# Kernel tuning notes

Hardware: AMD Instinct MI355X
Metric: run time of the kernel (lower is better)

## Reference

```python
import jax, jax.numpy as jnp
import numpy as np

# levels for the auction iterations: j = 7..-1 gives level = -4^j, j = -2 gives level = 0
_LEVEL_JS = list(range(7, -3, -1))


def approx_match(xyz1, xyz2):
    # xyz1: [B,N,3], xyz2: [B,M,3] -> soft match matrix [B,N,M]
    B, N, _ = xyz1.shape
    M = xyz2.shape[1]
    multiL = 1.0 if N >= M else float(M // N)
    multiR = float(N // M) if N >= M else 1.0
    # pairwise squared distances [B,N,M]
    d2 = jnp.sum((xyz1[:, :, None, :] - xyz2[:, None, :, :]) ** 2, axis=-1)
    levels = jnp.array([0.0 if j == -2 else -(4.0 ** j) for j in _LEVEL_JS],
                       dtype=xyz1.dtype)

    def step(carry, level):
        match, remainL, remainR = carry
        w = jnp.exp(level * d2) * remainR[:, None, :]                      # [B,N,M]
        # row-normalize to each left point's remaining mass
        w = w * (remainL / (jnp.sum(w, axis=2) + 1e-9))[:, :, None]
        # clip columns to right points' remaining capacity
        ss = jnp.sum(w, axis=1) + 1e-9                                     # [B,M]
        w = w * jnp.minimum(remainR / ss, 1.0)[:, None, :]
        match = match + w
        remainL = jnp.maximum(remainL - jnp.sum(w, axis=2), 0.0)
        remainR = jnp.maximum(remainR - jnp.sum(w, axis=1), 0.0)
        return (match, remainL, remainR), None

    init = (jnp.zeros_like(d2),
            jnp.full((B, N), multiL, dtype=d2.dtype),
            jnp.full((B, M), multiR, dtype=d2.dtype))
    (match, _, _), _ = jax.lax.scan(step, init, levels)
    return match


def match_cost(xyz1, xyz2, match):
    # cost[b] = sum_{k,l} match[b,k,l] * ||xyz1[b,k] - xyz2[b,l]||
    d = jnp.sqrt(jnp.sum((xyz1[:, :, None, :] - xyz2[:, None, :, :]) ** 2, axis=-1))
    return jnp.sum(match * d, axis=(1, 2))


def setup_inputs() -> dict:
    key = jax.random.key(0)
    k1, k2 = jax.random.split(key)
    B, N, M = 8, 2048, 2048
    input1 = jax.random.normal(k1, (B, N, 3), dtype=jnp.float32)
    input2 = jax.random.normal(k2, (B, M, 3), dtype=jnp.float32)
    return {"input1": input1, "input2": input2}


def reference(input1, input2):
    match = approx_match(input1, input2)
    return match_cost(input1, input2, match)
```

## Files before the change

kernel.cpp:

```cpp
#include <hip/hip_runtime.h>
#include <hip/hip_fp16.h>


#define BATCH 8
#define NPTS 2048
#define MPTS 2048
#define BLOCK 256
#define ROWS 16
#define BLOCKS_PER_BATCH 128
#define NSUB 8
#define SUBTGT (BLOCKS_PER_BATCH / NSUB)
#define NSYNC 21
#define PAD 16
#define SROW 17
#define LOG2E 1.44269504088896340736f

__device__ __forceinline__ float fast_exp2(float x) {
  return __builtin_amdgcn_exp2f(x);
}
__device__ __forceinline__ float fast_sqrt(float a) {
  return __builtin_amdgcn_sqrtf(a);
}
__device__ __forceinline__ float packh2(float c, float r) {
  __half2 h = __halves2half2(__float2half_rn(c), __float2half_rn(r));
  return __builtin_bit_cast(float, h);
}

__device__ __forceinline__ float cohLoad(const float* p) {
  return __hip_atomic_load((float*)p, __ATOMIC_RELAXED,
                           __HIP_MEMORY_SCOPE_AGENT);
}
__device__ __forceinline__ void cohStore(float* p, float v) {
  __hip_atomic_store(p, v, __ATOMIC_RELAXED, __HIP_MEMORY_SCOPE_AGENT);
}
__device__ __forceinline__ float4 cohLoad4(const float4* p) {
  const float* f = (const float*)p;
  return make_float4(cohLoad(f), cohLoad(f + 1), cohLoad(f + 2),
                     cohLoad(f + 3));
}

__device__ __forceinline__ void lds_barrier() {
  asm volatile("s_waitcnt lgkmcnt(0)" ::: "memory");
  __builtin_amdgcn_s_barrier();
  __builtin_amdgcn_sched_barrier(0);
}

__device__ __forceinline__ void batch_barrier(unsigned* base, int bid) {
  __syncthreads();
  if (threadIdx.x == 0) {
    __hip_atomic_fetch_add(base + (bid & (NSUB - 1)) * PAD, 1u,
                           __ATOMIC_RELAXED, __HIP_MEMORY_SCOPE_AGENT);
  }
  if (threadIdx.x < NSUB) {
    int guard = 0;
    while (__hip_atomic_load(base + threadIdx.x * PAD, __ATOMIC_RELAXED,
                             __HIP_MEMORY_SCOPE_AGENT) < (unsigned)SUBTGT) {
      __builtin_amdgcn_s_sleep(2);
      if (++guard > (1 << 22)) break;
    }
  }
  asm volatile("" ::: "memory");
  __syncthreads();
}

__device__ __forceinline__ void load8(const float4* q, int r0,
                                      float* x, float* y, float* z) {
  int b4 = (r0 >> 2) * 3;
  float4 q0 = q[b4], q1 = q[b4 + 1], q2 = q[b4 + 2];
  float4 q3 = q[b4 + 3], q4 = q[b4 + 4], q5 = q[b4 + 5];
  x[0] = q0.x; y[0] = q0.y; z[0] = q0.z;
  x[1] = q0.w; y[1] = q1.x; z[1] = q1.y;
  x[2] = q1.z; y[2] = q1.w; z[2] = q2.x;
  x[3] = q2.y; y[3] = q2.z; z[3] = q2.w;
  x[4] = q3.x; y[4] = q3.y; z[4] = q3.z;
  x[5] = q3.w; y[5] = q4.x; z[5] = q4.y;
  x[6] = q4.z; y[6] = q4.w; z[6] = q5.x;
  x[7] = q5.y; y[7] = q5.z; z[7] = q5.w;
}

__device__ __forceinline__ void sweep2T_fuse(
    float nc, int tid, int t0, const float4* q1, const float* rsG,
    float* wpB, const float4* sP, float4* sStage4, float* sRR) {
  const int m_idx = tid >> 4, c = tid & 15;
  const float4 pm = sP[t0 + m_idx];
  const float4* rsg4 = (const float4*)rsG;
  const int rowb = c * SROW;
  const bool isXyz = tid < 192;
  const int t = tid - 192;
  const int wIdx = isXyz ? ((tid / 12) * SROW + (tid % 12))
                         : ((t >> 2) * SROW + 12 + (t & 3));
  float4 v = isXyz ? q1[tid] : cohLoad4(rsg4 + t);
  float part = 0.f;
  for (int chunk = 0; chunk < 8; ++chunk) {
    lds_barrier();
    sStage4[wIdx] = v;
    if (chunk < 7) {
      v = isXyz ? q1[(chunk + 1) * 192 + tid]
                : cohLoad4(rsg4 + (chunk + 1) * 64 + t);
    }
    lds_barrier();
#pragma unroll
    for (int k = 0; k < 4; ++k) {
      float4 a  = sStage4[rowb + 3 * k];
      float4 bb = sStage4[rowb + 3 * k + 1];
      float4 cc = sStage4[rowb + 3 * k + 2];
      float4 r4 = sStage4[rowb + 12 + k];
      float px[4] = {a.x, a.w, bb.z, cc.y};
      float py[4] = {a.y, bb.x, bb.w, cc.z};
      float pz[4] = {a.z, bb.y, cc.x, cc.w};
      float rr[4] = {r4.x, r4.y, r4.z, r4.w};
#pragma unroll
      for (int j = 0; j < 4; ++j) {
        float dx = px[j] - pm.x, dy = py[j] - pm.y, dz = pz[j] - pm.z;
        float d2 = __builtin_fmaf(dx, dx, __builtin_fmaf(dy, dy, dz * dz));
        part = __builtin_fmaf(fast_exp2(nc * d2), rr[j], part);
      }
    }
  }
  part += __shfl_xor(part, 1, 64);
  part += __shfl_xor(part, 2, 64);
  part += __shfl_xor(part, 4, 64);
  part += __shfl_xor(part, 8, 64);
  if (c == 0) {
    float t1v = part;
    float rr = sRR[m_idx];
    float colsum = rr * t1v;
    float cs = fminf(rr / (colsum + 1e-9f), 1.0f);
    float ccv = rr * cs;
    float rn = fmaxf(rr - colsum * cs, 0.f);
    cohStore(wpB + t0 + m_idx, packh2(ccv, rn));
    sRR[m_idx] = rn;
  }
}

__global__ __launch_bounds__(BLOCK, 4) void emd_fused_kernel(
    const float* __restrict__ xyz1, const float* __restrict__ xyz2,
    float* __restrict__ out, float* __restrict__ rowscaleG,
    float* __restrict__ wPack, float* __restrict__ R9acc,
    float* __restrict__ t9, float* __restrict__ outAcc,
    unsigned* __restrict__ ctr) {
  __shared__ float4 sP[MPTS];
  __shared__ float4 sStage4[16 * SROW];
  __shared__ float sRedS[ROWS * 4];
  __shared__ float sRedC[ROWS * 4];
  __shared__ float sRedR[ROWS * 4];
  __shared__ float sCost[ROWS];
  __shared__ float sRowScale[ROWS];
  __shared__ float sRemainL[ROWS];
  __shared__ float sRR[ROWS];

  const int tid = threadIdx.x;
  const int bid = blockIdx.x;
  const int b = bid >> 7;
  const int t0 = (bid & 127) * ROWS;
  const bool desig = (bid & 127) == 0;
  const int wave = tid >> 6, lane = tid & 63;
  const size_t bM = (size_t)b * MPTS;
  float costAcc = 0.f;

  float* rsG = rowscaleG + (size_t)b * NPTS;
  float* wpB = wPack + bM;
  const float4* q1 = (const float4*)(xyz1 + (size_t)b * NPTS * 3);
  const float4* q2 = (const float4*)(xyz2 + bM * 3);
#define CTRB(s) (ctr + (size_t)(((s) * BATCH + b) * NSUB) * PAD)

  for (int g = tid; g < MPTS / 4; g += BLOCK) {
    float4 a = q2[3 * g], bb = q2[3 * g + 1], c = q2[3 * g + 2];
    sP[4 * g + 0] = make_float4(a.x, a.y, a.z, 0.f);
    sP[4 * g + 1] = make_float4(a.w, bb.x, bb.y, 0.f);
    sP[4 * g + 2] = make_float4(bb.z, bb.w, c.x, 0.f);
    sP[4 * g + 3] = make_float4(c.y, c.z, c.w, 0.f);
  }
  if (tid < ROWS) sRR[tid] = 1.0f;
  if (desig && tid == 0) {
    cohStore(R9acc + b * PAD, 0.f);
    cohStore(t9 + b * PAD, 0.f);
    cohStore(outAcc + b * PAD, 0.f);
  }
  __syncthreads();

  const float nc0 = -16384.0f * LOG2E;
  {
    const int ph = lane >> 1, rg = lane & 1;
    float x1a[8], y1a[8], z1a[8], acc[8];
    load8(q1, t0 + rg * 8, x1a, y1a, z1a);
#pragma unroll
    for (int j = 0; j < 8; ++j) acc[j] = 0.f;
    const int mb = wave * 512 + ph;
#pragma unroll 2
    for (int it = 0; it < 16; ++it) {
      float4 v = sP[mb + it * 32];
#pragma unroll
      for (int j = 0; j < 8; ++j) {
        float dx = x1a[j] - v.x, dy = y1a[j] - v.y, dz = z1a[j] - v.z;
        float d2 = __builtin_fmaf(dx, dx, __builtin_fmaf(dy, dy, dz * dz));
        acc[j] += fast_exp2(nc0 * d2);
      }
    }
#pragma unroll
    for (int j = 0; j < 8; ++j) {
      acc[j] += __shfl_xor(acc[j], 2, 64);
      acc[j] += __shfl_xor(acc[j], 4, 64);
      acc[j] += __shfl_xor(acc[j], 8, 64);
      acc[j] += __shfl_xor(acc[j], 16, 64);
      acc[j] += __shfl_xor(acc[j], 32, 64);
    }
    if (lane < 2) {
#pragma unroll
      for (int j = 0; j < 8; ++j) sRedS[(rg * 8 + j) * 4 + wave] = acc[j];
    }
    __syncthreads();
    if (tid < ROWS) {
      float s = sRedS[tid * 4] + sRedS[tid * 4 + 1] + sRedS[tid * 4 + 2] +
                sRedS[tid * 4 + 3];
      float rs = 1.0f / (s + 1e-9f);
      sRowScale[tid] = rs;
      cohStore(rsG + t0 + tid, rs);
    }
  }
  batch_barrier(CTRB(0), bid);
  sweep2T_fuse(nc0, tid, t0, q1, rsG, wpB, sP, sStage4, sRR);
  batch_barrier(CTRB(1), bid);

  float x1[4], y1[4], z1[4];
  {
    int b4 = ((t0 + (lane & 3) * 4) >> 2) * 3;
    float4 a = q1[b4], bb = q1[b4 + 1], c = q1[b4 + 2];
    x1[0] = a.x;  y1[0] = a.y;  z1[0] = a.z;
    x1[1] = a.w;  y1[1] = bb.x; z1[1] = bb.y;
    x1[2] = bb.z; y1[2] = bb.w; z1[2] = c.x;
    x1[3] = c.y;  y1[3] = c.z;  z1[3] = c.w;
  }
  const int phc = lane >> 2, rgc = lane & 3;
  const int mbc = wave * 512 + phc;

  float nc2 = -4096.0f * LOG2E;
  for (int l = 0; l < 9; ++l) {
    const bool LAST = (l == 8);
#pragma unroll
    for (int k = 0; k < 8; ++k) {
      int m = tid + k * 256;
      sP[m].w = cohLoad(wpB + m);
    }
    __syncthreads();
    float accS[4] = {0.f, 0.f, 0.f, 0.f};
    float accC[4] = {0.f, 0.f, 0.f, 0.f};
    float accR[4] = {0.f, 0.f, 0.f, 0.f};
#pragma unroll 4
    for (int it = 0; it < 32; ++it) {
      float4 v = sP[mbc + it * 16];
      __half2 h = __builtin_bit_cast(__half2, v.w);
      float cc = __low2float(h);
      float rr = __high2float(h);
#pragma unroll
      for (int j = 0; j < 4; ++j) {
        float dx = x1[j] - v.x, dy = y1[j] - v.y, dz = z1[j] - v.z;
        float d2 = __builtin_fmaf(dx, dx, __builtin_fmaf(dy, dy, dz * dz));
        float sq = fast_sqrt(d2);
        float e2 = fast_exp2(nc2 * d2);
        float e2s = e2 * e2;
        float e1 = e2s * e2s;
        float t = e1 * cc;
        accS[j] += t;
        accC[j] = __builtin_fmaf(t, sq, accC[j]);
        accR[j] = __builtin_fmaf(e2, rr, accR[j]);
      }
    }
#pragma unroll
    for (int j = 0; j < 4; ++j) {
      accS[j] += __shfl_xor(accS[j], 4, 64);
      accS[j] += __shfl_xor(accS[j], 8, 64);
      accS[j] += __shfl_xor(accS[j], 16, 64);
      accS[j] += __shfl_xor(accS[j], 32, 64);
      accC[j] += __shfl_xor(accC[j], 4, 64);
      accC[j] += __shfl_xor(accC[j], 8, 64);
      accC[j] += __shfl_xor(accC[j], 16, 64);
      accC[j] += __shfl_xor(accC[j], 32, 64);
      accR[j] += __shfl_xor(accR[j], 4, 64);
      accR[j] += __shfl_xor(accR[j], 8, 64);
      accR[j] += __shfl_xor(accR[j], 16, 64);
      accR[j] += __shfl_xor(accR[j], 32, 64);
    }
    if (lane < 4) {
#pragma unroll
      for (int j = 0; j < 4; ++j) {
        sRedS[(rgc * 4 + j) * 4 + wave] = accS[j];
        sRedC[(rgc * 4 + j) * 4 + wave] = accC[j];
        sRedR[(rgc * 4 + j) * 4 + wave] = accR[j];
      }
    }
    __syncthreads();
    if (tid < ROWS) {
      float S2 = sRedS[tid * 4] + sRedS[tid * 4 + 1] + sRedS[tid * 4 + 2] +
                 sRedS[tid * 4 + 3];
      float C = sRedC[tid * 4] + sRedC[tid * 4 + 1] + sRedC[tid * 4 + 2] +
                sRedC[tid * 4 + 3];
      float R = sRedR[tid * 4] + sRedR[tid * 4 + 1] + sRedR[tid * 4 + 2] +
                sRedR[tid * 4 + 3];
      if (LAST) R = cohLoad(R9acc + b * PAD);
      float rs = sRowScale[tid];
      float rl = (l == 0) ? 1.0f : sRemainL[tid];
      float rlN = fmaxf(rl - rs * S2, 0.f);
      sRemainL[tid] = rlN;
      float rsN = rlN / (R + 1e-9f);
      sRowScale[tid] = rsN;
      if (!LAST) cohStore(rsG + t0 + tid, rsN);
      sCost[tid] = rs * C;
    }
    __syncthreads();
    if (tid == 0) {
      float t = 0.f;
#pragma unroll
      for (int i = 0; i < ROWS; ++i) t += sCost[i];
      costAcc += t;
      if (LAST) {
        float r = 0.f;
#pragma unroll
        for (int i = 0; i < ROWS; ++i) r += sRowScale[i];
        atomicAdd(t9 + b * PAD, r);
      }
    }
    if (!LAST) {
      batch_barrier(CTRB(2 + 2 * l), bid);
      sweep2T_fuse(nc2, tid, t0, q1, rsG, wpB, sP, sStage4, sRR);
      if (l == 7) {
        __syncthreads();
        if (tid == 0) {
          float r9 = 0.f;
#pragma unroll
          for (int i = 0; i < ROWS; ++i) r9 += sRR[i];
          atomicAdd(R9acc + b * PAD, r9);
        }
      }
      batch_barrier(CTRB(3 + 2 * l), bid);
      nc2 *= 0.25f;
    }
  }
  batch_barrier(CTRB(18), bid);

  if (tid < ROWS) {
    float rr = sRR[tid];
    float t1s = cohLoad(t9 + b * PAD);
    float w = rr * fminf(rr / (__builtin_fmaf(rr, t1s, 1e-9f)), 1.0f);
    cohStore(wpB + t0 + tid, w);
  }
  batch_barrier(CTRB(19), bid);

  {
#pragma unroll
    for (int k = 0; k < 8; ++k) {
      int m = tid + k * 256;
      sP[m].w = cohLoad(wpB + m);
    }
    __syncthreads();
    const int ph = lane >> 1, rg = lane & 1;
    float x1a[8], y1a[8], z1a[8], acc[8];
    load8(q1, t0 + rg * 8, x1a, y1a, z1a);
#pragma unroll
    for (int j = 0; j < 8; ++j) acc[j] = 0.f;
    const int mb = wave * 512 + ph;
#pragma unroll 2
    for (int it = 0; it < 16; ++it) {
      float4 v = sP[mb + it * 32];
#pragma unroll
      for (int j = 0; j < 8; ++j) {
        float dx = x1a[j] - v.x, dy = y1a[j] - v.y, dz = z1a[j] - v.z;
        float d2 = __builtin_fmaf(dx, dx, __builtin_fmaf(dy, dy, dz * dz));
        acc[j] = __builtin_fmaf(fast_sqrt(d2), v.w, acc[j]);
      }
    }
#pragma unroll
    for (int j = 0; j < 8; ++j) {
      acc[j] += __shfl_xor(acc[j], 2, 64);
      acc[j] += __shfl_xor(acc[j], 4, 64);
      acc[j] += __shfl_xor(acc[j], 8, 64);
      acc[j] += __shfl_xor(acc[j], 16, 64);
      acc[j] += __shfl_xor(acc[j], 32, 64);
    }
    if (lane < 2) {
#pragma unroll
      for (int j = 0; j < 8; ++j) sRedS[(rg * 8 + j) * 4 + wave] = acc[j];
    }
    __syncthreads();
    if (tid < ROWS) {
      float C = sRedS[tid * 4] + sRedS[tid * 4 + 1] + sRedS[tid * 4 + 2] +
                sRedS[tid * 4 + 3];
      sCost[tid] = sRowScale[tid] * C;
    }
    __syncthreads();
    if (tid == 0) {
      float t = 0.f;
#pragma unroll
      for (int i = 0; i < ROWS; ++i) t += sCost[i];
      costAcc += t;
      atomicAdd(outAcc + b * PAD, costAcc);
    }
  }
  batch_barrier(CTRB(20), bid);
  if (desig && tid == 0) out[b] = cohLoad(outAcc + b * PAD);
#undef CTRB
}

extern "C" void kernel_launch(void* const* d_in, const int* in_sizes, int n_in,
                              void* d_out, int out_size, void* d_ws, size_t ws_size,
                              hipStream_t stream) {
  const float* xyz1 = (const float*)d_in[0];
  const float* xyz2 = (const float*)d_in[1];
  float* out = (float*)d_out;
  float* ws = (float*)d_ws;

  const int BM = BATCH * MPTS;
  float* rowscaleG = ws;
  float* wPack     = ws + BM;
  float* R9acc     = ws + 2 * BM;
  float* t9        = ws + 2 * BM + BATCH * PAD;
  float* outAcc    = ws + 2 * BM + 2 * BATCH * PAD;
  unsigned* ctr    = (unsigned*)(ws + 2 * BM + 3 * BATCH * PAD);

  hipMemsetAsync(ctr, 0, (size_t)NSYNC * BATCH * NSUB * PAD * sizeof(unsigned),
                 stream);

  void* args[] = {(void*)&xyz1, (void*)&xyz2, (void*)&out, (void*)&rowscaleG,
                  (void*)&wPack, (void*)&R9acc, (void*)&t9, (void*)&outAcc,
                  (void*)&ctr};
  hipLaunchKernel((const void*)emd_fused_kernel,
                  dim3(BATCH * (NPTS / ROWS)), dim3(BLOCK), args, 0, stream);
}
```

Measured before the change: 378.0 us.

## Double block size to 512 threads with 32 rows per block, halving blocks per batch

Each block now owns 32 rows with 512 threads. The eight waves are split into two row halves, each covering four column quarters. The column sweep processes two staged chunks per LDS round, which halves the loop trips. Blocks per batch fall from 128 to 64, so fewer blocks take part in each grid-wide batch barrier and there is less barrier and atomic traffic. The cost is fewer, larger blocks, so occupancy and load balance across CUs may suffer, and launch bounds of 4 blocks per CU at 512 threads may constrain registers.

```diff
diff --git a/kernel.cpp b/kernel.cpp
--- a/kernel.cpp
+++ b/kernel.cpp
@@ -5,9 +5,9 @@
 #define BATCH 8
 #define NPTS 2048
 #define MPTS 2048
-#define BLOCK 256
-#define ROWS 16
-#define BLOCKS_PER_BATCH 128
+#define BLOCK 512
+#define ROWS 32
+#define BLOCKS_PER_BATCH 64
 #define NSUB 8
 #define SUBTGT (BLOCKS_PER_BATCH / NSUB)
 #define NSYNC 21
@@ -80,40 +80,47 @@
 
 __device__ __forceinline__ void sweep2T_fuse(
     float nc, int tid, int t0, const float4* q1, const float* rsG,
-    float* wpB, const float4* sP, float4* sStage4, float* sRR) {
+    float* wpB, const float4* sP, float4* sStage, float* sRR) {
   const int m_idx = tid >> 4, c = tid & 15;
   const float4 pm = sP[t0 + m_idx];
   const float4* rsg4 = (const float4*)rsG;
   const int rowb = c * SROW;
-  const bool isXyz = tid < 192;
-  const int t = tid - 192;
-  const int wIdx = isXyz ? ((tid / 12) * SROW + (tid % 12))
-                         : ((t >> 2) * SROW + 12 + (t & 3));
-  float4 v = isXyz ? q1[tid] : cohLoad4(rsg4 + t);
+  const int tl = tid & 255;
+  const int half = tid >> 8;
+  const bool isXyz = tl < 192;
+  const int t = tl - 192;
+  const int wIdx = half * (16 * SROW) +
+                   (isXyz ? ((tl / 12) * SROW + (tl % 12))
+                          : ((t >> 2) * SROW + 12 + (t & 3)));
+  float4 v = isXyz ? q1[half * 192 + tl] : cohLoad4(rsg4 + half * 64 + t);
   float part = 0.f;
-  for (int chunk = 0; chunk < 8; ++chunk) {
+  for (int r = 0; r < 4; ++r) {
     lds_barrier();
-    sStage4[wIdx] = v;
-    if (chunk < 7) {
-      v = isXyz ? q1[(chunk + 1) * 192 + tid]
-                : cohLoad4(rsg4 + (chunk + 1) * 64 + t);
+    sStage[wIdx] = v;
+    if (r < 3) {
+      int ch = 2 * (r + 1) + half;
+      v = isXyz ? q1[ch * 192 + tl] : cohLoad4(rsg4 + ch * 64 + t);
     }
     lds_barrier();
 #pragma unroll
-    for (int k = 0; k < 4; ++k) {
-      float4 a  = sStage4[rowb + 3 * k];
-      float4 bb = sStage4[rowb + 3 * k + 1];
-      float4 cc = sStage4[rowb + 3 * k + 2];
-      float4 r4 = sStage4[rowb + 12 + k];
-      float px[4] = {a.x, a.w, bb.z, cc.y};
-      float py[4] = {a.y, bb.x, bb.w, cc.z};
-      float pz[4] = {a.z, bb.y, cc.x, cc.w};
-      float rr[4] = {r4.x, r4.y, r4.z, r4.w};
-#pragma unroll
-      for (int j = 0; j < 4; ++j) {
-        float dx = px[j] - pm.x, dy = py[j] - pm.y, dz = pz[j] - pm.z;
-        float d2 = __builtin_fmaf(dx, dx, __builtin_fmaf(dy, dy, dz * dz));
-        part = __builtin_fmaf(fast_exp2(nc * d2), rr[j], part);
+    for (int h = 0; h < 2; ++h) {
+      const float4* sB = sStage + h * (16 * SROW);
+#pragma unroll
+      for (int k = 0; k < 4; ++k) {
+        float4 a  = sB[rowb + 3 * k];
+        float4 bb = sB[rowb + 3 * k + 1];
+        float4 cc = sB[rowb + 3 * k + 2];
+        float4 r4 = sB[rowb + 12 + k];
+        float px[4] = {a.x, a.w, bb.z, cc.y};
+        float py[4] = {a.y, bb.x, bb.w, cc.z};
+        float pz[4] = {a.z, bb.y, cc.x, cc.w};
+        float rr[4] = {r4.x, r4.y, r4.z, r4.w};
+#pragma unroll
+        for (int j = 0; j < 4; ++j) {
+          float dx = px[j] - pm.x, dy = py[j] - pm.y, dz = pz[j] - pm.z;
+          float d2 = __builtin_fmaf(dx, dx, __builtin_fmaf(dy, dy, dz * dz));
+          part = __builtin_fmaf(fast_exp2(nc * d2), rr[j], part);
+        }
       }
     }
   }
@@ -140,7 +147,7 @@
     float* __restrict__ t9, float* __restrict__ outAcc,
     unsigned* __restrict__ ctr) {
   __shared__ float4 sP[MPTS];
-  __shared__ float4 sStage4[16 * SROW];
+  __shared__ float4 sStage[2 * 16 * SROW];
   __shared__ float sRedS[ROWS * 4];
   __shared__ float sRedC[ROWS * 4];
   __shared__ float sRedR[ROWS * 4];
@@ -151,10 +158,12 @@
 
   const int tid = threadIdx.x;
   const int bid = blockIdx.x;
-  const int b = bid >> 7;
-  const int t0 = (bid & 127) * ROWS;
-  const bool desig = (bid & 127) == 0;
+  const int b = bid >> 6;
+  const int t0 = (bid & 63) * ROWS;
+  const bool desig = (bid & 63) == 0;
   const int wave = tid >> 6, lane = tid & 63;
+  const int mq = wave & 3;
+  const int rh = wave >> 2;
   const size_t bM = (size_t)b * MPTS;
   float costAcc = 0.f;
 
@@ -164,7 +173,8 @@
   const float4* q2 = (const float4*)(xyz2 + bM * 3);
 #define CTRB(s) (ctr + (size_t)(((s) * BATCH + b) * NSUB) * PAD)
 
-  for (int g = tid; g < MPTS / 4; g += BLOCK) {
+  {
+    int g = tid;
     float4 a = q2[3 * g], bb = q2[3 * g + 1], c = q2[3 * g + 2];
     sP[4 * g + 0] = make_float4(a.x, a.y, a.z, 0.f);
     sP[4 * g + 1] = make_float4(a.w, bb.x, bb.y, 0.f);
@@ -183,10 +193,10 @@
   {
     const int ph = lane >> 1, rg = lane & 1;
     float x1a[8], y1a[8], z1a[8], acc[8];
-    load8(q1, t0 + rg * 8, x1a, y1a, z1a);
+    load8(q1, t0 + rh * 16 + rg * 8, x1a, y1a, z1a);
 #pragma unroll
     for (int j = 0; j < 8; ++j) acc[j] = 0.f;
-    const int mb = wave * 512 + ph;
+    const int mb = mq * 512 + ph;
 #pragma unroll 2
     for (int it = 0; it < 16; ++it) {
       float4 v = sP[mb + it * 32];
@@ -207,7 +217,8 @@
     }
     if (lane < 2) {
 #pragma unroll
-      for (int j = 0; j < 8; ++j) sRedS[(rg * 8 + j) * 4 + wave] = acc[j];
+      for (int j = 0; j < 8; ++j)
+        sRedS[(rh * 16 + rg * 8 + j) * 4 + mq] = acc[j];
     }
     __syncthreads();
     if (tid < ROWS) {
@@ -219,12 +230,12 @@
     }
   }
   batch_barrier(CTRB(0), bid);
-  sweep2T_fuse(nc0, tid, t0, q1, rsG, wpB, sP, sStage4, sRR);
+  sweep2T_fuse(nc0, tid, t0, q1, rsG, wpB, sP, sStage, sRR);
   batch_barrier(CTRB(1), bid);
 
   float x1[4], y1[4], z1[4];
   {
-    int b4 = ((t0 + (lane & 3) * 4) >> 2) * 3;
+    int b4 = ((t0 + rh * 16 + (lane & 3) * 4) >> 2) * 3;
     float4 a = q1[b4], bb = q1[b4 + 1], c = q1[b4 + 2];
     x1[0] = a.x;  y1[0] = a.y;  z1[0] = a.z;
     x1[1] = a.w;  y1[1] = bb.x; z1[1] = bb.y;
@@ -232,14 +243,14 @@
     x1[3] = c.y;  y1[3] = c.z;  z1[3] = c.w;
   }
   const int phc = lane >> 2, rgc = lane & 3;
-  const int mbc = wave * 512 + phc;
+  const int mbc = mq * 512 + phc;
 
   float nc2 = -4096.0f * LOG2E;
   for (int l = 0; l < 9; ++l) {
     const bool LAST = (l == 8);
 #pragma unroll
-    for (int k = 0; k < 8; ++k) {
-      int m = tid + k * 256;
+    for (int k = 0; k < 4; ++k) {
+      int m = tid + k * 512;
       sP[m].w = cohLoad(wpB + m);
     }
     __syncthreads();
@@ -284,9 +295,10 @@
     if (lane < 4) {
 #pragma unroll
       for (int j = 0; j < 4; ++j) {
-        sRedS[(rgc * 4 + j) * 4 + wave] = accS[j];
-        sRedC[(rgc * 4 + j) * 4 + wave] = accC[j];
-        sRedR[(rgc * 4 + j) * 4 + wave] = accR[j];
+        int row = rh * 16 + rgc * 4 + j;
+        sRedS[row * 4 + mq] = accS[j];
+        sRedC[row * 4 + mq] = accC[j];
+        sRedR[row * 4 + mq] = accR[j];
       }
     }
     __syncthreads();
@@ -322,7 +334,7 @@
     }
     if (!LAST) {
       batch_barrier(CTRB(2 + 2 * l), bid);
-      sweep2T_fuse(nc2, tid, t0, q1, rsG, wpB, sP, sStage4, sRR);
+      sweep2T_fuse(nc2, tid, t0, q1, rsG, wpB, sP, sStage, sRR);
       if (l == 7) {
         __syncthreads();
         if (tid == 0) {
@@ -348,17 +360,17 @@
 
   {
 #pragma unroll
-    for (int k = 0; k < 8; ++k) {
-      int m = tid + k * 256;
+    for (int k = 0; k < 4; ++k) {
+      int m = tid + k * 512;
       sP[m].w = cohLoad(wpB + m);
     }
     __syncthreads();
     const int ph = lane >> 1, rg = lane & 1;
     float x1a[8], y1a[8], z1a[8], acc[8];
-    load8(q1, t0 + rg * 8, x1a, y1a, z1a);
+    load8(q1, t0 + rh * 16 + rg * 8, x1a, y1a, z1a);
 #pragma unroll
     for (int j = 0; j < 8; ++j) acc[j] = 0.f;
-    const int mb = wave * 512 + ph;
+    const int mb = mq * 512 + ph;
 #pragma unroll 2
     for (int it = 0; it < 16; ++it) {
       float4 v = sP[mb + it * 32];
@@ -379,7 +391,8 @@
     }
     if (lane < 2) {
 #pragma unroll
-      for (int j = 0; j < 8; ++j) sRedS[(rg * 8 + j) * 4 + wave] = acc[j];
+      for (int j = 0; j < 8; ++j)
+        sRedS[(rh * 16 + rg * 8 + j) * 4 + mq] = acc[j];
     }
     __syncthreads();
     if (tid < ROWS) {
```

Result: faster. 314.6 us (-16.8%).
